# Performance work log

Hardware: AMD Instinct MI355X
Metric: run time of the kernel (lower is better)

## Reference

```python
import jax, jax.numpy as jnp
import numpy as np

N = 65536
WAVE_SPEED = 1.0


def _mlp(pt, Ws, bs):
    # pt: [4] -> scalar. 6 tanh hidden layers of width 128, linear head.
    h = pt
    for W, b in zip(Ws[:-1], bs[:-1]):
        h = jnp.tanh(W @ h + b)
    return (Ws[-1] @ h + bs[-1])[0]


def setup_inputs() -> dict:
    key = jax.random.key(0)
    ks = jax.random.split(key, 32)
    d = {}
    for i, name in enumerate(["t", "x", "y", "z"]):
        d[name] = jax.random.normal(ks[i], (N,), dtype=jnp.float32)
    sizes = [(128, 4)] + [(128, 128)] * 5 + [(1, 128)]
    for i, (fan_out, fan_in) in enumerate(sizes):
        # Glorot-like scale for tanh MLP
        scale = np.float32(1.0 / np.sqrt(fan_in))
        d[f"W{i}"] = jax.random.normal(ks[4 + i], (fan_out, fan_in), dtype=jnp.float32) * scale
        d[f"b{i}"] = jnp.zeros((fan_out,), dtype=jnp.float32)
    return d


def reference(t, x, y, z, W0, b0, W1, b1, W2, b2, W3, b3, W4, b4, W5, b5, W6, b6):
    Ws = [W0, W1, W2, W3, W4, W5, W6]
    bs = [b0, b1, b2, b3, b4, b5, b6]

    def u(pt):
        return _mlp(pt, Ws, bs)

    def residual_point(pt):
        # Full 4x4 Hessian via forward-over-reverse; we need only the diagonal.
        H = jax.hessian(u)(pt)  # [4, 4]
        u_tt = H[0, 0]
        laplacian = H[1, 1] + H[2, 2] + H[3, 3]
        return u_tt - (WAVE_SPEED ** 2) * laplacian

    pts = jnp.stack([t, x, y, z], axis=-1)  # [N, 4]
    return jax.vmap(residual_point)(pts)  # [N]
```

## Files before the change

kernel.cpp:

```cpp
#include <hip/hip_runtime.h>
#include <hip/hip_fp16.h>
#include <math.h>


typedef _Float16 f16x8 __attribute__((ext_vector_type(8)));
typedef _Float16 f16x4 __attribute__((ext_vector_type(4)));
typedef _Float16 f16x2 __attribute__((ext_vector_type(2)));
typedef float    f32x4 __attribute__((ext_vector_type(4)));

constexpr int TPB  = 256;
constexpr int P    = 16;
constexpr int H    = 128;
constexpr int XPAD = 136;
constexpr int NV   = 6;
constexpr int WFRAG_HALVES = 5 * 8 * 4 * 64 * 8;
constexpr size_t WS_NEEDED = 2 * WFRAG_HALVES * sizeof(_Float16);

__device__ __forceinline__ float fast_tanh(float v) {
    float e = __expf(-2.0f * fabsf(v));
    float r = __builtin_amdgcn_rcpf(1.0f + e);
    return copysignf((1.0f - e) * r, v);
}

__device__ __forceinline__ f16x2 pkrtz(float a, float b) {
    return __builtin_bit_cast(f16x2, __builtin_amdgcn_cvt_pkrtz(a, b));
}

__global__ __launch_bounds__(TPB) void presplit_w(
    const float* __restrict__ W1, const float* __restrict__ W2,
    const float* __restrict__ W3, const float* __restrict__ W4,
    const float* __restrict__ W5, _Float16* __restrict__ whi,
    _Float16* __restrict__ wlo)
{
    const int gid = blockIdx.x * TPB + threadIdx.x;
    const float* Ws[5] = { W1, W2, W3, W4, W5 };
    const int lane = gid & 63;
    const int rest = gid >> 6;
    const int ks   = rest & 3;
    const int mt   = (rest >> 2) & 7;
    const int l    = rest >> 5;
    const int n    = mt * 16 + (lane & 15);
    const int k0   = ks * 32 + (lane >> 4) * 8;
    const float4 u0 = *(const float4*)&Ws[l][n * H + k0];
    const float4 u1 = *(const float4*)&Ws[l][n * H + k0 + 4];
    const float vv[8] = { u0.x, u0.y, u0.z, u0.w, u1.x, u1.y, u1.z, u1.w };
    f16x8 h, o;
    #pragma unroll
    for (int e = 0; e < 8; ++e) {
        _Float16 hh = (_Float16)vv[e];
        h[e] = hh;
        o[e] = (_Float16)(vv[e] - (float)hh);
    }
    *(f16x8*)&whi[gid * 8] = h;
    *(f16x8*)&wlo[gid * 8] = o;
}

__global__ __launch_bounds__(TPB, 3) void pinn_mfma3(
    const float* __restrict__ t, const float* __restrict__ x,
    const float* __restrict__ y, const float* __restrict__ z,
    const float* __restrict__ W0, const float* __restrict__ b0,
    const float* __restrict__ W1, const float* __restrict__ b1,
    const float* __restrict__ W2, const float* __restrict__ b2,
    const float* __restrict__ W3, const float* __restrict__ b3,
    const float* __restrict__ W4, const float* __restrict__ b4,
    const float* __restrict__ W5, const float* __restrict__ b5,
    const float* __restrict__ W6,
    const _Float16* __restrict__ whi, const _Float16* __restrict__ wlo,
    int use_pre, float* __restrict__ out, int N)
{
    __shared__ _Float16 sXhi[NV * P * XPAD];
    __shared__ _Float16 sXlo[NV * P * XPAD];
    __shared__ float    sRed[4][P];

    const int tid  = threadIdx.x;
    const int lane = tid & 63;
    const int wn   = tid >> 6;
    const int l15  = lane & 15;
    const int l4   = lane >> 4;
    const int gb   = blockIdx.x * P;

    {
        const int p0 = tid >> 4;
        const int i0 = tid & 15;
        int gp = gb + p0; if (gp >= N) gp = N - 1;
        const float pt0 = t[gp], pt1 = x[gp], pt2 = y[gp], pt3 = z[gp];
        float nv[NV][8];
        #pragma unroll
        for (int j = 0; j < 8; ++j) {
            const int i = i0 * 8 + j;
            const float4 wv = *(const float4*)&W0[i * 4];
            const float zv = fmaf(wv.x, pt0, fmaf(wv.y, pt1, fmaf(wv.z, pt2, fmaf(wv.w, pt3, b0[i]))));
            const float hv = fast_tanh(zv);
            const float s  = 1.0f - hv * hv;
            const float ssq = ((wv.x * wv.x - wv.y * wv.y) - wv.z * wv.z) - wv.w * wv.w;
            nv[0][j] = hv;       nv[1][j] = s * wv.x; nv[2][j] = s * wv.y;
            nv[3][j] = s * wv.z; nv[4][j] = s * wv.w; nv[5][j] = -2.0f * hv * s * ssq;
        }
        #pragma unroll
        for (int v = 0; v < NV; ++v) {
            f16x8 hh, oo;
            #pragma unroll
            for (int j = 0; j < 8; ++j) {
                _Float16 h_ = (_Float16)nv[v][j];
                hh[j] = h_;
                oo[j] = (_Float16)(nv[v][j] - (float)h_);
            }
            const int off = (v * P + p0) * XPAD + i0 * 8;
            *(f16x8*)&sXhi[off] = hh;
            *(f16x8*)&sXlo[off] = oo;
        }
    }
    __syncthreads();

    const float* Wl[5] = { W1, W2, W3, W4, W5 };
    const float* bl[5] = { b1, b2, b3, b4, b5 };

    for (int l = 0; l < 5; ++l) {
        f16x8 ah[2][4], al[2][4];
        if (use_pre) {
            #pragma unroll
            for (int nt = 0; nt < 2; ++nt)
                #pragma unroll
                for (int ks = 0; ks < 4; ++ks) {
                    const int f = ((l * 8 + (wn * 2 + nt)) * 4 + ks) * 64 + lane;
                    ah[nt][ks] = *(const f16x8*)&whi[f * 8];
                    al[nt][ks] = *(const f16x8*)&wlo[f * 8];
                }
        } else {
            const float* __restrict__ Wc = Wl[l];
            #pragma unroll
            for (int nt = 0; nt < 2; ++nt)
                #pragma unroll
                for (int ks = 0; ks < 4; ++ks) {
                    const int n  = (wn * 2 + nt) * 16 + l15;
                    const int k0 = ks * 32 + l4 * 8;
                    const float4 u0 = *(const float4*)&Wc[n * H + k0];
                    const float4 u1 = *(const float4*)&Wc[n * H + k0 + 4];
                    const float vv[8] = { u0.x, u0.y, u0.z, u0.w, u1.x, u1.y, u1.z, u1.w };
                    #pragma unroll
                    for (int e = 0; e < 8; ++e) {
                        _Float16 h_ = (_Float16)vv[e];
                        ah[nt][ks][e] = h_;
                        al[nt][ks][e] = (_Float16)(vv[e] - (float)h_);
                    }
                }
        }

        f32x4 acc[NV][2];
        #pragma unroll
        for (int v = 0; v < NV; ++v)
            #pragma unroll
            for (int nt = 0; nt < 2; ++nt) acc[v][nt] = (f32x4){0.f, 0.f, 0.f, 0.f};

        #pragma unroll
        for (int ks = 0; ks < 4; ++ks) {
            f16x8 xh[NV], xl[NV];
            #pragma unroll
            for (int v = 0; v < NV; ++v) {
                const int base = (v * P + l15) * XPAD + ks * 32 + l4 * 8;
                xh[v] = *(const f16x8*)&sXhi[base];
                xl[v] = *(const f16x8*)&sXlo[base];
            }
            __builtin_amdgcn_s_setprio(1);
            #pragma unroll
            for (int v = 0; v < NV; ++v)
                #pragma unroll
                for (int nt = 0; nt < 2; ++nt)
                    acc[v][nt] = __builtin_amdgcn_mfma_f32_16x16x32_f16(ah[nt][ks], xh[v], acc[v][nt], 0, 0, 0);
            #pragma unroll
            for (int v = 0; v < NV; ++v)
                #pragma unroll
                for (int nt = 0; nt < 2; ++nt)
                    acc[v][nt] = __builtin_amdgcn_mfma_f32_16x16x32_f16(ah[nt][ks], xl[v], acc[v][nt], 0, 0, 0);
            #pragma unroll
            for (int v = 0; v < NV; ++v)
                #pragma unroll
                for (int nt = 0; nt < 2; ++nt)
                    acc[v][nt] = __builtin_amdgcn_mfma_f32_16x16x32_f16(al[nt][ks], xh[v], acc[v][nt], 0, 0, 0);
            __builtin_amdgcn_s_setprio(0);
        }
        __syncthreads();

        if (l < 4) {
            const float* __restrict__ bc = bl[l];
            #pragma unroll
            for (int nt = 0; nt < 2; ++nt) {
                const int n0 = (wn * 2 + nt) * 16 + l4 * 4;
                const float4 b4v = *(const float4*)&bc[n0];
                const float bb[4] = { b4v.x, b4v.y, b4v.z, b4v.w };
                float nv[NV][4];
                #pragma unroll
                for (int r = 0; r < 4; ++r) {
                    const float zv = acc[0][nt][r] + bb[r];
                    const float hv = fast_tanh(zv);
                    const float s  = 1.0f - hv * hv;
                    const float d0 = acc[1][nt][r], d1 = acc[2][nt][r];
                    const float d2 = acc[3][nt][r], d3 = acc[4][nt][r];
                    const float ssq = ((d0 * d0 - d1 * d1) - d2 * d2) - d3 * d3;
                    const float qn  = fmaf(s, acc[5][nt][r], -2.0f * hv * s * ssq);
                    nv[0][r] = hv;     nv[1][r] = s * d0; nv[2][r] = s * d1;
                    nv[3][r] = s * d2; nv[4][r] = s * d3; nv[5][r] = qn;
                }
                #pragma unroll
                for (int v = 0; v < NV; ++v) {
                    const f16x2 h01 = pkrtz(nv[v][0], nv[v][1]);
                    const f16x2 h23 = pkrtz(nv[v][2], nv[v][3]);
                    const float o0 = nv[v][0] - (float)h01[0];
                    const float o1 = nv[v][1] - (float)h01[1];
                    const float o2 = nv[v][2] - (float)h23[0];
                    const float o3 = nv[v][3] - (float)h23[1];
                    const f16x2 o01 = pkrtz(o0, o1);
                    const f16x2 o23 = pkrtz(o2, o3);
                    const int off = (v * P + l15) * XPAD + n0;
                    *(f16x4*)&sXhi[off] = __builtin_shufflevector(h01, h23, 0, 1, 2, 3);
                    *(f16x4*)&sXlo[off] = __builtin_shufflevector(o01, o23, 0, 1, 2, 3);
                }
            }
            __syncthreads();
        } else {
            const float* __restrict__ bc = bl[4];
            float part = 0.0f;
            #pragma unroll
            for (int nt = 0; nt < 2; ++nt) {
                const int n0 = (wn * 2 + nt) * 16 + l4 * 4;
                const float4 b4v = *(const float4*)&bc[n0];
                const float4 w6v = *(const float4*)&W6[n0];
                const float bb[4] = { b4v.x, b4v.y, b4v.z, b4v.w };
                const float ww[4] = { w6v.x, w6v.y, w6v.z, w6v.w };
                #pragma unroll
                for (int r = 0; r < 4; ++r) {
                    const float zv = acc[0][nt][r] + bb[r];
                    const float hv = fast_tanh(zv);
                    const float s  = 1.0f - hv * hv;
                    const float d0 = acc[1][nt][r], d1 = acc[2][nt][r];
                    const float d2 = acc[3][nt][r], d3 = acc[4][nt][r];
                    const float ssq = ((d0 * d0 - d1 * d1) - d2 * d2) - d3 * d3;
                    const float qf  = fmaf(s, acc[5][nt][r], -2.0f * hv * s * ssq);
                    part = fmaf(ww[r], qf, part);
                }
            }
            part += __shfl_xor(part, 16, 64);
            part += __shfl_xor(part, 32, 64);
            if (lane < 16) sRed[wn][lane] = part;
        }
    }

    __syncthreads();
    if (tid < P) {
        const float rsum = sRed[0][tid] + sRed[1][tid] + sRed[2][tid] + sRed[3][tid];
        const int o = gb + tid;
        if (o < N) out[o] = rsum;
    }
}

extern "C" void kernel_launch(void* const* d_in, const int* in_sizes, int n_in,
                              void* d_out, int out_size, void* d_ws, size_t ws_size,
                              hipStream_t stream) {
    const float* t  = (const float*)d_in[0];
    const float* x  = (const float*)d_in[1];
    const float* y  = (const float*)d_in[2];
    const float* z  = (const float*)d_in[3];
    const float* W0 = (const float*)d_in[4];
    const float* b0 = (const float*)d_in[5];
    const float* W1 = (const float*)d_in[6];
    const float* b1 = (const float*)d_in[7];
    const float* W2 = (const float*)d_in[8];
    const float* b2 = (const float*)d_in[9];
    const float* W3 = (const float*)d_in[10];
    const float* b3 = (const float*)d_in[11];
    const float* W4 = (const float*)d_in[12];
    const float* b4 = (const float*)d_in[13];
    const float* W5 = (const float*)d_in[14];
    const float* b5 = (const float*)d_in[15];
    const float* W6 = (const float*)d_in[16];

    const int N = in_sizes[0];
    float* out = (float*)d_out;

    const int use_pre = (ws_size >= WS_NEEDED) ? 1 : 0;
    _Float16* whi = (_Float16*)d_ws;
    _Float16* wlo = whi + WFRAG_HALVES;

    if (use_pre) {
        presplit_w<<<(5 * 8 * 4 * 64) / TPB, TPB, 0, stream>>>(W1, W2, W3, W4, W5, whi, wlo);
    }
    const int grid = (N + P - 1) / P;
    pinn_mfma3<<<grid, TPB, 0, stream>>>(
        t, x, y, z, W0, b0, W1, b1, W2, b2, W3, b3, W4, b4, W5, b5, W6,
        whi, wlo, use_pre, out, N);
}
```

Measured before the change: 213.4 us.

## Use two waves per block with four M-tiles each and per-k-step weight loads

Halves the block to 128 threads so each wave covers four 16-row output tiles instead of two. Weight fragments are now loaded per k-step inside the loop rather than all up front. Each loaded activation fragment from LDS now feeds twice as many MFMAs, which cuts LDS read traffic per block. The cost is more accumulator registers per wave (6x4 f32x4 tiles) and a lower occupancy bound of 2, so latency hiding may suffer.

```diff
diff --git a/kernel.cpp b/kernel.cpp
--- a/kernel.cpp
+++ b/kernel.cpp
@@ -8,11 +8,12 @@
 typedef _Float16 f16x2 __attribute__((ext_vector_type(2)));
 typedef float    f32x4 __attribute__((ext_vector_type(4)));
 
-constexpr int TPB  = 256;
+constexpr int TPB  = 128;
 constexpr int P    = 16;
 constexpr int H    = 128;
 constexpr int XPAD = 136;
 constexpr int NV   = 6;
+constexpr int NMT  = 4;
 constexpr int WFRAG_HALVES = 5 * 8 * 4 * 64 * 8;
 constexpr size_t WS_NEEDED = 2 * WFRAG_HALVES * sizeof(_Float16);
 
@@ -26,13 +27,13 @@
     return __builtin_bit_cast(f16x2, __builtin_amdgcn_cvt_pkrtz(a, b));
 }
 
-__global__ __launch_bounds__(TPB) void presplit_w(
+__global__ __launch_bounds__(128) void presplit_w(
     const float* __restrict__ W1, const float* __restrict__ W2,
     const float* __restrict__ W3, const float* __restrict__ W4,
     const float* __restrict__ W5, _Float16* __restrict__ whi,
     _Float16* __restrict__ wlo)
 {
-    const int gid = blockIdx.x * TPB + threadIdx.x;
+    const int gid = blockIdx.x * 128 + threadIdx.x;
     const float* Ws[5] = { W1, W2, W3, W4, W5 };
     const int lane = gid & 63;
     const int rest = gid >> 6;
@@ -55,7 +56,7 @@
     *(f16x8*)&wlo[gid * 8] = o;
 }
 
-__global__ __launch_bounds__(TPB, 3) void pinn_mfma3(
+__global__ __launch_bounds__(TPB, 2) void pinn_mfma4(
     const float* __restrict__ t, const float* __restrict__ x,
     const float* __restrict__ y, const float* __restrict__ z,
     const float* __restrict__ W0, const float* __restrict__ b0,
@@ -70,44 +71,47 @@
 {
     __shared__ _Float16 sXhi[NV * P * XPAD];
     __shared__ _Float16 sXlo[NV * P * XPAD];
-    __shared__ float    sRed[4][P];
+    __shared__ float    sRed[2][P];
 
     const int tid  = threadIdx.x;
     const int lane = tid & 63;
-    const int wn   = tid >> 6;
+    const int w    = tid >> 6;
     const int l15  = lane & 15;
     const int l4   = lane >> 4;
     const int gb   = blockIdx.x * P;
 
     {
-        const int p0 = tid >> 4;
-        const int i0 = tid & 15;
+        const int p0 = tid >> 3;
+        const int i0 = tid & 7;
         int gp = gb + p0; if (gp >= N) gp = N - 1;
         const float pt0 = t[gp], pt1 = x[gp], pt2 = y[gp], pt3 = z[gp];
-        float nv[NV][8];
         #pragma unroll
-        for (int j = 0; j < 8; ++j) {
-            const int i = i0 * 8 + j;
-            const float4 wv = *(const float4*)&W0[i * 4];
-            const float zv = fmaf(wv.x, pt0, fmaf(wv.y, pt1, fmaf(wv.z, pt2, fmaf(wv.w, pt3, b0[i]))));
-            const float hv = fast_tanh(zv);
-            const float s  = 1.0f - hv * hv;
-            const float ssq = ((wv.x * wv.x - wv.y * wv.y) - wv.z * wv.z) - wv.w * wv.w;
-            nv[0][j] = hv;       nv[1][j] = s * wv.x; nv[2][j] = s * wv.y;
-            nv[3][j] = s * wv.z; nv[4][j] = s * wv.w; nv[5][j] = -2.0f * hv * s * ssq;
-        }
-        #pragma unroll
-        for (int v = 0; v < NV; ++v) {
-            f16x8 hh, oo;
+        for (int pass = 0; pass < 2; ++pass) {
+            float nv[NV][8];
             #pragma unroll
             for (int j = 0; j < 8; ++j) {
-                _Float16 h_ = (_Float16)nv[v][j];
-                hh[j] = h_;
-                oo[j] = (_Float16)(nv[v][j] - (float)h_);
-            }
-            const int off = (v * P + p0) * XPAD + i0 * 8;
-            *(f16x8*)&sXhi[off] = hh;
-            *(f16x8*)&sXlo[off] = oo;
+                const int i = i0 * 16 + pass * 8 + j;
+                const float4 wv = *(const float4*)&W0[i * 4];
+                const float zv = fmaf(wv.x, pt0, fmaf(wv.y, pt1, fmaf(wv.z, pt2, fmaf(wv.w, pt3, b0[i]))));
+                const float hv = fast_tanh(zv);
+                const float s  = 1.0f - hv * hv;
+                const float ssq = ((wv.x * wv.x - wv.y * wv.y) - wv.z * wv.z) - wv.w * wv.w;
+                nv[0][j] = hv;       nv[1][j] = s * wv.x; nv[2][j] = s * wv.y;
+                nv[3][j] = s * wv.z; nv[4][j] = s * wv.w; nv[5][j] = -2.0f * hv * s * ssq;
+            }
+            #pragma unroll
+            for (int v = 0; v < NV; ++v) {
+                f16x8 hh, oo;
+                #pragma unroll
+                for (int j = 0; j < 8; ++j) {
+                    _Float16 h_ = (_Float16)nv[v][j];
+                    hh[j] = h_;
+                    oo[j] = (_Float16)(nv[v][j] - (float)h_);
+                }
+                const int off = (v * P + p0) * XPAD + i0 * 16 + pass * 8;
+                *(f16x8*)&sXhi[off] = hh;
+                *(f16x8*)&sXlo[off] = oo;
+            }
         }
     }
     __syncthreads();
@@ -116,23 +120,28 @@
     const float* bl[5] = { b1, b2, b3, b4, b5 };
 
     for (int l = 0; l < 5; ++l) {
-        f16x8 ah[2][4], al[2][4];
-        if (use_pre) {
-            #pragma unroll
-            for (int nt = 0; nt < 2; ++nt)
-                #pragma unroll
-                for (int ks = 0; ks < 4; ++ks) {
-                    const int f = ((l * 8 + (wn * 2 + nt)) * 4 + ks) * 64 + lane;
-                    ah[nt][ks] = *(const f16x8*)&whi[f * 8];
-                    al[nt][ks] = *(const f16x8*)&wlo[f * 8];
-                }
-        } else {
-            const float* __restrict__ Wc = Wl[l];
-            #pragma unroll
-            for (int nt = 0; nt < 2; ++nt)
-                #pragma unroll
-                for (int ks = 0; ks < 4; ++ks) {
-                    const int n  = (wn * 2 + nt) * 16 + l15;
+        f32x4 acc[NV][NMT];
+        #pragma unroll
+        for (int v = 0; v < NV; ++v)
+            #pragma unroll
+            for (int nt = 0; nt < NMT; ++nt) acc[v][nt] = (f32x4){0.f, 0.f, 0.f, 0.f};
+
+        const float* __restrict__ Wc = Wl[l];
+
+        #pragma unroll
+        for (int ks = 0; ks < 4; ++ks) {
+            f16x8 ah[NMT], al[NMT];
+            if (use_pre) {
+                #pragma unroll
+                for (int nt = 0; nt < NMT; ++nt) {
+                    const int f = ((l * 8 + (w * NMT + nt)) * 4 + ks) * 64 + lane;
+                    ah[nt] = *(const f16x8*)&whi[f * 8];
+                    al[nt] = *(const f16x8*)&wlo[f * 8];
+                }
+            } else {
+                #pragma unroll
+                for (int nt = 0; nt < NMT; ++nt) {
+                    const int n  = (w * NMT + nt) * 16 + l15;
                     const int k0 = ks * 32 + l4 * 8;
                     const float4 u0 = *(const float4*)&Wc[n * H + k0];
                     const float4 u1 = *(const float4*)&Wc[n * H + k0 + 4];
@@ -140,20 +149,11 @@
                     #pragma unroll
                     for (int e = 0; e < 8; ++e) {
                         _Float16 h_ = (_Float16)vv[e];
-                        ah[nt][ks][e] = h_;
-                        al[nt][ks][e] = (_Float16)(vv[e] - (float)h_);
+                        ah[nt][e] = h_;
+                        al[nt][e] = (_Float16)(vv[e] - (float)h_);
                     }
                 }
-        }
-
-        f32x4 acc[NV][2];
-        #pragma unroll
-        for (int v = 0; v < NV; ++v)
-            #pragma unroll
-            for (int nt = 0; nt < 2; ++nt) acc[v][nt] = (f32x4){0.f, 0.f, 0.f, 0.f};
-
-        #pragma unroll
-        for (int ks = 0; ks < 4; ++ks) {
+            }
             f16x8 xh[NV], xl[NV];
             #pragma unroll
             for (int v = 0; v < NV; ++v) {
@@ -165,18 +165,18 @@
             #pragma unroll
             for (int v = 0; v < NV; ++v)
                 #pragma unroll
-                for (int nt = 0; nt < 2; ++nt)
-                    acc[v][nt] = __builtin_amdgcn_mfma_f32_16x16x32_f16(ah[nt][ks], xh[v], acc[v][nt], 0, 0, 0);
+                for (int nt = 0; nt < NMT; ++nt)
+                    acc[v][nt] = __builtin_amdgcn_mfma_f32_16x16x32_f16(ah[nt], xh[v], acc[v][nt], 0, 0, 0);
             #pragma unroll
             for (int v = 0; v < NV; ++v)
                 #pragma unroll
-                for (int nt = 0; nt < 2; ++nt)
-                    acc[v][nt] = __builtin_amdgcn_mfma_f32_16x16x32_f16(ah[nt][ks], xl[v], acc[v][nt], 0, 0, 0);
+                for (int nt = 0; nt < NMT; ++nt)
+                    acc[v][nt] = __builtin_amdgcn_mfma_f32_16x16x32_f16(ah[nt], xl[v], acc[v][nt], 0, 0, 0);
             #pragma unroll
             for (int v = 0; v < NV; ++v)
                 #pragma unroll
-                for (int nt = 0; nt < 2; ++nt)
-                    acc[v][nt] = __builtin_amdgcn_mfma_f32_16x16x32_f16(al[nt][ks], xh[v], acc[v][nt], 0, 0, 0);
+                for (int nt = 0; nt < NMT; ++nt)
+                    acc[v][nt] = __builtin_amdgcn_mfma_f32_16x16x32_f16(al[nt], xh[v], acc[v][nt], 0, 0, 0);
             __builtin_amdgcn_s_setprio(0);
         }
         __syncthreads();
@@ -184,8 +184,8 @@
         if (l < 4) {
             const float* __restrict__ bc = bl[l];
             #pragma unroll
-            for (int nt = 0; nt < 2; ++nt) {
-                const int n0 = (wn * 2 + nt) * 16 + l4 * 4;
+            for (int nt = 0; nt < NMT; ++nt) {
+                const int n0 = (w * NMT + nt) * 16 + l4 * 4;
                 const float4 b4v = *(const float4*)&bc[n0];
                 const float bb[4] = { b4v.x, b4v.y, b4v.z, b4v.w };
                 float nv[NV][4];
@@ -221,8 +221,8 @@
             const float* __restrict__ bc = bl[4];
             float part = 0.0f;
             #pragma unroll
-            for (int nt = 0; nt < 2; ++nt) {
-                const int n0 = (wn * 2 + nt) * 16 + l4 * 4;
+            for (int nt = 0; nt < NMT; ++nt) {
+                const int n0 = (w * NMT + nt) * 16 + l4 * 4;
                 const float4 b4v = *(const float4*)&bc[n0];
                 const float4 w6v = *(const float4*)&W6[n0];
                 const float bb[4] = { b4v.x, b4v.y, b4v.z, b4v.w };
@@ -241,13 +241,13 @@
             }
             part += __shfl_xor(part, 16, 64);
             part += __shfl_xor(part, 32, 64);
-            if (lane < 16) sRed[wn][lane] = part;
+            if (lane < 16) sRed[w][lane] = part;
         }
     }
 
     __syncthreads();
     if (tid < P) {
-        const float rsum = sRed[0][tid] + sRed[1][tid] + sRed[2][tid] + sRed[3][tid];
+        const float rsum = sRed[0][tid] + sRed[1][tid];
         const int o = gb + tid;
         if (o < N) out[o] = rsum;
     }
@@ -282,10 +282,10 @@
     _Float16* wlo = whi + WFRAG_HALVES;
 
     if (use_pre) {
-        presplit_w<<<(5 * 8 * 4 * 64) / TPB, TPB, 0, stream>>>(W1, W2, W3, W4, W5, whi, wlo);
+        presplit_w<<<(5 * 8 * 4 * 64) / 128, 128, 0, stream>>>(W1, W2, W3, W4, W5, whi, wlo);
     }
     const int grid = (N + P - 1) / P;
-    pinn_mfma3<<<grid, TPB, 0, stream>>>(
+    pinn_mfma4<<<grid, TPB, 0, stream>>>(
         t, x, y, z, W0, b0, W1, b1, W2, b2, W3, b3, W4, b4, W5, b5, W6,
         whi, wlo, use_pre, out, N);
 }
```

Result: slower. 225.6 us (+5.7%).
